# Performance work log

Measured on AMD Instinct MI355X. Metric: run time of the kernel, lower is better.

The kernel has to match this reference:

```python
import jax, jax.numpy as jnp
import numpy as np

TEMPERATURE = 2.0

def setup_inputs() -> dict:
    key = jax.random.key(0)
    x = jax.random.normal(key, (8192, 512), dtype=jnp.float32)
    return {"x": x}

def reference(x) -> jnp.ndarray:
    # torch.pdist(x, p=2).pow(2) == squared euclidean distance over pairs i<j
    n = x.shape[0]
    sq = jnp.sum(x * x, axis=1)                       # [N]
    d2 = sq[:, None] + sq[None, :] - 2.0 * (x @ x.T)  # [N, N]
    d2 = jnp.maximum(d2, 0.0)                         # numerical clamp
    mask = jnp.triu(jnp.ones((n, n), dtype=jnp.bool_), k=1)  # strict upper tri = pdist pairs
    num_pairs = n * (n - 1) // 2
    e = jnp.where(mask, jnp.exp(-TEMPERATURE * d2), 0.0)
    return jnp.log(jnp.sum(e) / num_pairs)
```

## Files before the change

### kernel.cpp

```cpp
#include <hip/hip_runtime.h>
#include <hip/hip_fp8.h>
#include <math.h>

#define N 8192
#define D 512
#define NEG_INF_SENT (-3.0e38f)
#define SCALE1 0x7F7F7F7F

typedef __attribute__((ext_vector_type(8))) int int8x;
typedef __attribute__((ext_vector_type(16))) float f32x16;

#define AS1 __attribute__((address_space(1)))
#define AS3 __attribute__((address_space(3)))

__device__ inline void lse_merge(float& m1, float& s1, float m2, float s2) {
    float M = fmaxf(m1, m2);
    s1 = s1 * __expf(m1 - M) + s2 * __expf(m2 - M);
    m1 = M;
}

__global__ __launch_bounds__(256) void cast_rowsq_kernel(const float* __restrict__ x,
                                                         unsigned char* __restrict__ xb,
                                                         float* __restrict__ sq) {
#pragma unroll
    for (int g4 = 0; g4 < 4; ++g4) {
        int row = blockIdx.x * 16 + g4 * 4 + (threadIdx.x >> 6);
        int lane = threadIdx.x & 63;
        const float4* xr = (const float4*)(x + (size_t)row * D);
        float4 a = xr[lane * 2], b = xr[lane * 2 + 1];
        float v[8] = {a.x, a.y, a.z, a.w, b.x, b.y, b.z, b.w};
        float s = 0.f;
        unsigned int byt[8];
#pragma unroll
        for (int e = 0; e < 8; ++e) {
            s += v[e] * v[e];
            __hip_fp8_e4m3 f8(v[e]);
            byt[e] = (unsigned int)f8.__x;
        }
        uint2 pk;
        pk.x = byt[0] | (byt[1] << 8) | (byt[2] << 16) | (byt[3] << 24);
        pk.y = byt[4] | (byt[5] << 8) | (byt[6] << 16) | (byt[7] << 24);
        int g = row >> 5, rl = row & 31;
        int c = lane >> 3;
        int l5 = (lane >> 2) & 1;
        int h = (lane >> 1) & 1;
        int bb = (lane & 1) << 3;
        size_t addr = ((size_t)((g * 8 + c) * 2 + h) << 10) + ((l5 * 32 + rl) << 4) + bb;
        *(uint2*)(xb + addr) = pk;
#pragma unroll
        for (int off = 32; off > 0; off >>= 1) s += __shfl_down(s, off, 64);
        if (lane == 0) sq[row] = s;
    }
}

__global__ __launch_bounds__(512, 2) void pair_mfma_kernel(const unsigned char* __restrict__ xb,
                                                           const float* __restrict__ sq,
                                                           float* __restrict__ bm,
                                                           float* __restrict__ bs) {
    __shared__ __align__(16) unsigned char lds[2][16][2048];

    const int T = N / 256;
    const int b = (blockIdx.x & 7) * 66 + (blockIdx.x >> 3);
    int bi = 0;
    while ((bi + 1) * (2 * T - bi) / 2 <= b) ++bi;
    const int bj = bi + (b - bi * (2 * T - bi + 1) / 2);
    const int i0 = bi * 256, j0 = bj * 256;

    const int tid = threadIdx.x;
    const int lane = tid & 63;
    const int w = tid >> 6;
    const int wy = w >> 1;
    const int wx = w & 1;
    const int l31 = lane & 31;
    const int l5 = lane >> 5;
    const int f0 = w << 1;
    const int gA = i0 >> 5, gB = j0 >> 5;

    f32x16 acc[2][4];
#pragma unroll
    for (int mi = 0; mi < 2; ++mi)
#pragma unroll
        for (int ni = 0; ni < 4; ++ni)
#pragma unroll
            for (int r = 0; r < 16; ++r) acc[mi][ni][r] = 0.f;

    auto stage = [&](int c, int buf) {
#pragma unroll
        for (int q = 0; q < 2; ++q) {
            int f = f0 + q;
            int grp = (f < 8) ? (gA + f) : (gB + (f - 8));
            const unsigned char* src = xb + ((size_t)((grp * 8 + c) * 2) << 10);
#pragma unroll
            for (int h = 0; h < 2; ++h)
                __builtin_amdgcn_global_load_lds(
                    (const AS1 void*)(src + (h << 10)),
                    (AS3 void*)&lds[buf][f][h << 10], 16, 0, 0);
        }
    };

    stage(0, 0);
    __syncthreads();

    for (int c = 0; c < 8; ++c) {
        const int cur = c & 1;
        if (c < 7) stage(c + 1, cur ^ 1);
        int8x af[2], bf[4];
#pragma unroll
        for (int mi = 0; mi < 2; ++mi) {
            uint4 lo = *(const uint4*)&lds[cur][wy * 2 + mi][lane << 4];
            uint4 hi = *(const uint4*)&lds[cur][wy * 2 + mi][1024 + (lane << 4)];
            af[mi][0] = lo.x; af[mi][1] = lo.y; af[mi][2] = lo.z; af[mi][3] = lo.w;
            af[mi][4] = hi.x; af[mi][5] = hi.y; af[mi][6] = hi.z; af[mi][7] = hi.w;
        }
#pragma unroll
        for (int ni = 0; ni < 4; ++ni) {
            uint4 lo = *(const uint4*)&lds[cur][8 + wx * 4 + ni][lane << 4];
            uint4 hi = *(const uint4*)&lds[cur][8 + wx * 4 + ni][1024 + (lane << 4)];
            bf[ni][0] = lo.x; bf[ni][1] = lo.y; bf[ni][2] = lo.z; bf[ni][3] = lo.w;
            bf[ni][4] = hi.x; bf[ni][5] = hi.y; bf[ni][6] = hi.z; bf[ni][7] = hi.w;
        }
#pragma unroll
        for (int mi = 0; mi < 2; ++mi)
#pragma unroll
            for (int ni = 0; ni < 4; ++ni)
                acc[mi][ni] = __builtin_amdgcn_mfma_scale_f32_32x32x64_f8f6f4(
                    af[mi], bf[ni], acc[mi][ni], 0, 0, 0, SCALE1, 0, SCALE1);
        __syncthreads();
    }

    const bool offdiag = (bi != bj);
    float sqj[4];
#pragma unroll
    for (int ni = 0; ni < 4; ++ni) sqj[ni] = sq[j0 + wx * 128 + ni * 32 + l31];

    float m = NEG_INF_SENT;
#pragma unroll
    for (int mi = 0; mi < 2; ++mi) {
#pragma unroll
        for (int r = 0; r < 16; ++r) {
            int row32 = (r & 3) + 8 * (r >> 2) + 4 * l5;
            int i = i0 + wy * 64 + mi * 32 + row32;
            float sqi = sq[i];
#pragma unroll
            for (int ni = 0; ni < 4; ++ni) {
                int j = j0 + wx * 128 + ni * 32 + l31;
                float d2 = fmaxf(sqi + sqj[ni] - 2.f * acc[mi][ni][r], 0.f);
                float tv = (offdiag || j > i) ? (-2.0f * d2) : NEG_INF_SENT;
                acc[mi][ni][r] = tv;
                m = fmaxf(m, tv);
            }
        }
    }
    float s = 0.f;
#pragma unroll
    for (int mi = 0; mi < 2; ++mi)
#pragma unroll
        for (int ni = 0; ni < 4; ++ni)
#pragma unroll
            for (int r = 0; r < 16; ++r)
                s += __expf(acc[mi][ni][r] - m);

#pragma unroll
    for (int off = 32; off > 0; off >>= 1) {
        float m2 = __shfl_down(m, off, 64);
        float s2 = __shfl_down(s, off, 64);
        lse_merge(m, s, m2, s2);
    }
    __shared__ float rm[8], rs[8];
    if (lane == 0) { rm[w] = m; rs[w] = s; }
    __syncthreads();
    if (tid == 0) {
#pragma unroll
        for (int v = 1; v < 8; ++v) lse_merge(rm[0], rs[0], rm[v], rs[v]);
        bm[b] = rm[0];
        bs[b] = rs[0];
    }
}

__global__ __launch_bounds__(256) void finalize_kernel(const float* __restrict__ bm,
                                                       const float* __restrict__ bs,
                                                       int nblocks,
                                                       float* __restrict__ out) {
    const int tid = threadIdx.x;
    float m = NEG_INF_SENT, s = 0.f;
    for (int b = tid; b < nblocks; b += 256) lse_merge(m, s, bm[b], bs[b]);
#pragma unroll
    for (int off = 32; off > 0; off >>= 1) {
        float m2 = __shfl_down(m, off, 64);
        float s2 = __shfl_down(s, off, 64);
        lse_merge(m, s, m2, s2);
    }
    __shared__ float rm[4], rs[4];
    if ((tid & 63) == 0) { rm[tid >> 6] = m; rs[tid >> 6] = s; }
    __syncthreads();
    if (tid == 0) {
#pragma unroll
        for (int v = 1; v < 4; ++v) lse_merge(rm[0], rs[0], rm[v], rs[v]);
        const float log_num_pairs = 17.3285362f;
        out[0] = rm[0] + logf(rs[0]) - log_num_pairs;
    }
}

extern "C" void kernel_launch(void* const* d_in, const int* in_sizes, int n_in,
                              void* d_out, int out_size, void* d_ws, size_t ws_size,
                              hipStream_t stream) {
    const float* x = (const float*)d_in[0];
    float* out = (float*)d_out;

    const int T = N / 256;
    const int nb = T * (T + 1) / 2;
    const size_t xb_bytes = (size_t)N * D;

    unsigned char* xb = (unsigned char*)d_ws;
    float* sq = (float*)((char*)d_ws + xb_bytes);
    float* bm = sq + N;
    float* bs = bm + nb;

    cast_rowsq_kernel<<<N / 16, 256, 0, stream>>>(x, xb, sq);
    pair_mfma_kernel<<<nb, 512, 0, stream>>>(xb, sq, bm, bs);
    finalize_kernel<<<1, 256, 0, stream>>>(bm, bs, nb, out);
}
```

Before: 99.19 us.

## Shrink pair tiles to 128x128 with 256-thread blocks for more parallelism

Changes the triangular tile decomposition from 256x256 tiles (528 blocks, 512 threads) to 128x128 tiles (2080 blocks, 256 threads), with 4 waves each computing a 64x64 sub-tile. The staging and LDS layout are reworked to load 32 1KB fragments per k-chunk over 4 double-buffered chunks. The aim is better load balance and occupancy across CUs with less diagonal-tile waste, at the cost of lower operand reuse per block and more global/LDS traffic per FLOP.

```diff
diff --git a/kernel.cpp b/kernel.cpp
--- a/kernel.cpp
+++ b/kernel.cpp
@@ -4,6 +4,8 @@
 
 #define N 8192
 #define D 512
+#define TT 64
+#define NT 2080
 #define NEG_INF_SENT (-3.0e38f)
 #define SCALE1 0x7F7F7F7F
 
@@ -53,85 +55,91 @@
     }
 }
 
-__global__ __launch_bounds__(512, 2) void pair_mfma_kernel(const unsigned char* __restrict__ xb,
+__global__ __launch_bounds__(256, 2) void pair_mfma_kernel(const unsigned char* __restrict__ xb,
                                                            const float* __restrict__ sq,
                                                            float* __restrict__ bm,
                                                            float* __restrict__ bs) {
-    __shared__ __align__(16) unsigned char lds[2][16][2048];
-
-    const int T = N / 256;
-    const int b = (blockIdx.x & 7) * 66 + (blockIdx.x >> 3);
+    __shared__ __align__(16) unsigned char lds[2][32][1024];
+
+    const int p = blockIdx.x;
+    const int b = (p & 7) * 260 + (p >> 3);
     int bi = 0;
-    while ((bi + 1) * (2 * T - bi) / 2 <= b) ++bi;
-    const int bj = bi + (b - bi * (2 * T - bi + 1) / 2);
-    const int i0 = bi * 256, j0 = bj * 256;
+    while ((bi + 1) * (2 * TT - bi) / 2 <= b) ++bi;
+    const int bj = bi + (b - bi * (2 * TT - bi + 1) / 2);
+    const int i0 = bi * 128, j0 = bj * 128;
+    const int gA = i0 >> 5, gB = j0 >> 5;
 
     const int tid = threadIdx.x;
     const int lane = tid & 63;
     const int w = tid >> 6;
-    const int wy = w >> 1;
-    const int wx = w & 1;
+    const int wy = w >> 1, wx = w & 1;
     const int l31 = lane & 31;
     const int l5 = lane >> 5;
-    const int f0 = w << 1;
-    const int gA = i0 >> 5, gB = j0 >> 5;
-
-    f32x16 acc[2][4];
+
+    f32x16 acc[2][2];
 #pragma unroll
     for (int mi = 0; mi < 2; ++mi)
 #pragma unroll
-        for (int ni = 0; ni < 4; ++ni)
+        for (int ni = 0; ni < 2; ++ni)
 #pragma unroll
             for (int r = 0; r < 16; ++r) acc[mi][ni][r] = 0.f;
 
-    auto stage = [&](int c, int buf) {
-#pragma unroll
-        for (int q = 0; q < 2; ++q) {
-            int f = f0 + q;
-            int grp = (f < 8) ? (gA + f) : (gB + (f - 8));
-            const unsigned char* src = xb + ((size_t)((grp * 8 + c) * 2) << 10);
-#pragma unroll
-            for (int h = 0; h < 2; ++h)
-                __builtin_amdgcn_global_load_lds(
-                    (const AS1 void*)(src + (h << 10)),
-                    (AS3 void*)&lds[buf][f][h << 10], 16, 0, 0);
+    auto stage = [&](int C, int buf) {
+#pragma unroll
+        for (int u = 0; u < 8; ++u) {
+            int f = (w << 3) | u;
+            int side = f >> 4;
+            int g = (f >> 2) & 3;
+            int cc = (f >> 1) & 1;
+            int h = f & 1;
+            int grp = (side ? gB : gA) + g;
+            int cg = C * 2 + cc;
+            const unsigned char* src = xb + (((size_t)((grp * 8 + cg) * 2 + h)) << 10)
+                                          + (lane << 4);
+            __builtin_amdgcn_global_load_lds((const AS1 void*)src,
+                                             (AS3 void*)&lds[buf][f][0], 16, 0, 0);
         }
     };
 
     stage(0, 0);
     __syncthreads();
 
-    for (int c = 0; c < 8; ++c) {
-        const int cur = c & 1;
-        if (c < 7) stage(c + 1, cur ^ 1);
-        int8x af[2], bf[4];
-#pragma unroll
-        for (int mi = 0; mi < 2; ++mi) {
-            uint4 lo = *(const uint4*)&lds[cur][wy * 2 + mi][lane << 4];
-            uint4 hi = *(const uint4*)&lds[cur][wy * 2 + mi][1024 + (lane << 4)];
-            af[mi][0] = lo.x; af[mi][1] = lo.y; af[mi][2] = lo.z; af[mi][3] = lo.w;
-            af[mi][4] = hi.x; af[mi][5] = hi.y; af[mi][6] = hi.z; af[mi][7] = hi.w;
-        }
-#pragma unroll
-        for (int ni = 0; ni < 4; ++ni) {
-            uint4 lo = *(const uint4*)&lds[cur][8 + wx * 4 + ni][lane << 4];
-            uint4 hi = *(const uint4*)&lds[cur][8 + wx * 4 + ni][1024 + (lane << 4)];
-            bf[ni][0] = lo.x; bf[ni][1] = lo.y; bf[ni][2] = lo.z; bf[ni][3] = lo.w;
-            bf[ni][4] = hi.x; bf[ni][5] = hi.y; bf[ni][6] = hi.z; bf[ni][7] = hi.w;
-        }
-#pragma unroll
-        for (int mi = 0; mi < 2; ++mi)
-#pragma unroll
-            for (int ni = 0; ni < 4; ++ni)
-                acc[mi][ni] = __builtin_amdgcn_mfma_scale_f32_32x32x64_f8f6f4(
-                    af[mi], bf[ni], acc[mi][ni], 0, 0, 0, SCALE1, 0, SCALE1);
+    for (int C = 0; C < 4; ++C) {
+        const int cur = C & 1;
+        if (C < 3) stage(C + 1, cur ^ 1);
+#pragma unroll
+        for (int cc = 0; cc < 2; ++cc) {
+            int8x af[2], bf[2];
+#pragma unroll
+            for (int mi = 0; mi < 2; ++mi) {
+                int f = ((wy * 2 + mi) << 2) | (cc << 1);
+                uint4 lo = *(const uint4*)&lds[cur][f][lane << 4];
+                uint4 hi = *(const uint4*)&lds[cur][f + 1][lane << 4];
+                af[mi][0] = lo.x; af[mi][1] = lo.y; af[mi][2] = lo.z; af[mi][3] = lo.w;
+                af[mi][4] = hi.x; af[mi][5] = hi.y; af[mi][6] = hi.z; af[mi][7] = hi.w;
+            }
+#pragma unroll
+            for (int ni = 0; ni < 2; ++ni) {
+                int f = 16 | ((wx * 2 + ni) << 2) | (cc << 1);
+                uint4 lo = *(const uint4*)&lds[cur][f][lane << 4];
+                uint4 hi = *(const uint4*)&lds[cur][f + 1][lane << 4];
+                bf[ni][0] = lo.x; bf[ni][1] = lo.y; bf[ni][2] = lo.z; bf[ni][3] = lo.w;
+                bf[ni][4] = hi.x; bf[ni][5] = hi.y; bf[ni][6] = hi.z; bf[ni][7] = hi.w;
+            }
+#pragma unroll
+            for (int mi = 0; mi < 2; ++mi)
+#pragma unroll
+                for (int ni = 0; ni < 2; ++ni)
+                    acc[mi][ni] = __builtin_amdgcn_mfma_scale_f32_32x32x64_f8f6f4(
+                        af[mi], bf[ni], acc[mi][ni], 0, 0, 0, SCALE1, 0, SCALE1);
+        }
         __syncthreads();
     }
 
     const bool offdiag = (bi != bj);
-    float sqj[4];
-#pragma unroll
-    for (int ni = 0; ni < 4; ++ni) sqj[ni] = sq[j0 + wx * 128 + ni * 32 + l31];
+    float sqj[2];
+#pragma unroll
+    for (int ni = 0; ni < 2; ++ni) sqj[ni] = sq[j0 + wx * 64 + ni * 32 + l31];
 
     float m = NEG_INF_SENT;
 #pragma unroll
@@ -142,8 +150,8 @@
             int i = i0 + wy * 64 + mi * 32 + row32;
             float sqi = sq[i];
 #pragma unroll
-            for (int ni = 0; ni < 4; ++ni) {
-                int j = j0 + wx * 128 + ni * 32 + l31;
+            for (int ni = 0; ni < 2; ++ni) {
+                int j = j0 + wx * 64 + ni * 32 + l31;
                 float d2 = fmaxf(sqi + sqj[ni] - 2.f * acc[mi][ni][r], 0.f);
                 float tv = (offdiag || j > i) ? (-2.0f * d2) : NEG_INF_SENT;
                 acc[mi][ni][r] = tv;
@@ -155,7 +163,7 @@
 #pragma unroll
     for (int mi = 0; mi < 2; ++mi)
 #pragma unroll
-        for (int ni = 0; ni < 4; ++ni)
+        for (int ni = 0; ni < 2; ++ni)
 #pragma unroll
             for (int r = 0; r < 16; ++r)
                 s += __expf(acc[mi][ni][r] - m);
@@ -166,14 +174,14 @@
         float s2 = __shfl_down(s, off, 64);
         lse_merge(m, s, m2, s2);
     }
-    __shared__ float rm[8], rs[8];
+    __shared__ float rm[4], rs[4];
     if (lane == 0) { rm[w] = m; rs[w] = s; }
     __syncthreads();
     if (tid == 0) {
 #pragma unroll
-        for (int v = 1; v < 8; ++v) lse_merge(rm[0], rs[0], rm[v], rs[v]);
-        bm[b] = rm[0];
-        bs[b] = rs[0];
+        for (int v = 1; v < 4; ++v) lse_merge(rm[0], rs[0], rm[v], rs[v]);
+        bm[p] = rm[0];
+        bs[p] = rs[0];
     }
 }
 
@@ -207,16 +215,13 @@
     const float* x = (const float*)d_in[0];
     float* out = (float*)d_out;
 
-    const int T = N / 256;
-    const int nb = T * (T + 1) / 2;
     const size_t xb_bytes = (size_t)N * D;
-
     unsigned char* xb = (unsigned char*)d_ws;
     float* sq = (float*)((char*)d_ws + xb_bytes);
     float* bm = sq + N;
-    float* bs = bm + nb;
+    float* bs = bm + NT;
 
     cast_rowsq_kernel<<<N / 16, 256, 0, stream>>>(x, xb, sq);
-    pair_mfma_kernel<<<nb, 512, 0, stream>>>(xb, sq, bm, bs);
-    finalize_kernel<<<1, 256, 0, stream>>>(bm, bs, nb, out);
-}
+    pair_mfma_kernel<<<NT, 256, 0, stream>>>(xb, sq, bm, bs);
+    finalize_kernel<<<1, 256, 0, stream>>>(bm, bs, NT, out);
+}
```

Measured after the change: 103.9 us. 1.05x slower.
